# Kernel optimization log

Measured on AMD Instinct MI355X. Metric: run time of the kernel, lower is better.

## Reference

```python
import jax, jax.numpy as jnp
import numpy as np


def setup_inputs() -> dict:
    key = jax.random.key(0)
    ks = jax.random.split(key, 5)
    B, N, Fin, Fout = 8, 2048, 512, 512
    stdv = 1.0 / np.sqrt(Fout)
    w_stdv = 1.0 / np.sqrt(Fin)
    x = jax.random.normal(ks[0], (B, N, Fin), dtype=jnp.float32)
    weight = jax.random.uniform(ks[1], (Fin, Fout), dtype=jnp.float32, minval=-stdv, maxval=stdv)
    bias = jax.random.uniform(ks[2], (Fout,), dtype=jnp.float32, minval=-stdv, maxval=stdv)
    w_one = jax.random.uniform(ks[3], (Fin, Fin), dtype=jnp.float32, minval=-w_stdv, maxval=w_stdv)
    w_two = jax.random.uniform(ks[4], (Fin, Fin), dtype=jnp.float32, minval=-w_stdv, maxval=w_stdv)
    return {"x": x, "weight": weight, "bias": bias, "w_one": w_one, "w_two": w_two}


def reference(x, weight, bias, w_one, w_two):
    # x: [B, N, Fin]
    support = jnp.einsum('bnf,fo->bno', x, weight)          # [B, N, Fout]
    phi_one = jnp.einsum('ef,bnf->ben', w_one, x)           # [B, Fin, N]
    phi_two = jnp.einsum('ef,bnf->ben', w_two, x)           # [B, Fin, N]
    adj = jnp.einsum('ben,bem->bnm', phi_one, phi_two)      # [B, N, N]
    adj = jax.nn.softmax(adj, axis=1)                        # softmax over dim=1 (columns)
    out = jnp.einsum('bnm,bmo->bno', adj, support)           # [B, N, Fout]
    return out + bias
```

## Files before the change

### kernel.cpp

```cpp
#include <hip/hip_runtime.h>
#include <math.h>

#define BB 8
#define NN 2048
#define FF 512
#define LOG2E 1.4426950408889634f

typedef __attribute__((ext_vector_type(8))) short short8;
typedef __attribute__((ext_vector_type(4))) float floatx4;
typedef __attribute__((ext_vector_type(2))) float float2v;
typedef __attribute__((ext_vector_type(2))) __bf16 bf16x2;

__device__ __forceinline__ unsigned short f2bf(float f) {
    union { float f; unsigned u; } v; v.f = f;
    unsigned r = v.u + 0x7FFFu + ((v.u >> 16) & 1u);
    return (unsigned short)(r >> 16);
}

__device__ __forceinline__ float fexp2(float x) {
#if __has_builtin(__builtin_amdgcn_exp2f)
    return __builtin_amdgcn_exp2f(x);
#else
    return __expf(x * 0.69314718056f);
#endif
}

__device__ __forceinline__ void pk_store(unsigned short* p0, unsigned short* p1,
                                         float a, float b) {
    union { bf16x2 h; unsigned short s[2]; } u;
    float2v v; v.x = a; v.y = b;
    u.h = __builtin_convertvector(v, bf16x2);
    *p0 = u.s[0]; *p1 = u.s[1];
}

#define BAR() __builtin_amdgcn_s_barrier()
#define LGKM0() do { asm volatile("s_waitcnt lgkmcnt(0)" ::: "memory"); \
                     __builtin_amdgcn_sched_barrier(0); } while (0)
#define GLDS(src, dst) __builtin_amdgcn_global_load_lds( \
    (const __attribute__((address_space(1))) void*)(src), \
    (__attribute__((address_space(3))) void*)(dst), 16, 0, 0)
#define VMW(n) asm volatile("s_waitcnt vmcnt(" #n ")" ::: "memory")

template<int MODE>
__global__ __launch_bounds__(512) void gemm256(
    const unsigned short* __restrict__ A, const unsigned short* __restrict__ B,
    void* __restrict__ Cv, const float* __restrict__ bias, float* __restrict__ Dsum,
    int K, int a_ld, int b_ld, int ldc,
    long a_batch, long b_batch, long c_batch)
{
    constexpr int SLOT = 256 * 32;
    __shared__ __align__(16) unsigned short SH[8 * SLOT];

    const int tid  = threadIdx.x;
    const int wave = tid >> 6;
    const int lane = tid & 63;
    const int wr   = wave >> 2;
    const int wc   = wave & 3;
    const int fl   = lane & 15;
    const int quad = lane >> 4;

    const int gx = gridDim.x, gy = gridDim.y;
    int flat = blockIdx.x + gx * (blockIdx.y + gy * blockIdx.z);
    const int cpx = (gx * gy * gridDim.z) >> 3;
    flat = (flat & 7) * cpx + (flat >> 3);
    const int bx = flat % gx;
    const int rest = flat / gx;
    const int by = rest % gy;
    const int bz = rest / gy;

    const int m0 = by * 256;
    const int n0 = bx * 256;

    const unsigned short* Aptr = A + (long)bz * a_batch + (long)m0 * a_ld;
    const unsigned short* Bptr = B + (long)bz * b_batch + (long)n0 * b_ld;

    int offA[2], offB[2];
    #pragma unroll
    for (int i = 0; i < 2; ++i) {
        const int cl = i * 512 + tid;
        const int r = cl >> 2, s = cl & 3;
        const int c = s ^ ((r >> 1) & 3);
        offA[i] = r * a_ld + c * 8;
        offB[i] = r * b_ld + c * 8;
    }

    const int swz = (quad ^ ((fl >> 1) & 3)) * 8;
    const int aRd = (wr * 128 + fl) * 32 + swz;
    const int bRd = (wc * 64 + fl) * 32 + swz;

    auto sA = [&](int kh, int db, int kb) {
        #pragma unroll
        for (int i = 0; i < 2; ++i)
            GLDS(Aptr + kb + offA[i], &SH[(kh * 2 + db) * SLOT + (i * 512 + tid) * 8]);
    };
    auto sB = [&](int kh, int db, int kb) {
        #pragma unroll
        for (int i = 0; i < 2; ++i)
            GLDS(Bptr + kb + offB[i], &SH[(4 + kh * 2 + db) * SLOT + (i * 512 + tid) * 8]);
    };

    floatx4 acc[8][4] = {};
    short8 af[8], bf[2];

    auto RA = [&](int kh, int db) {
        const unsigned short* b = &SH[(kh * 2 + db) * SLOT + aRd];
        #pragma unroll
        for (int m = 0; m < 8; ++m) af[m] = *(const short8*)(b + m * 512);
    };
    auto RB = [&](int kh, int db, int nh) {
        const unsigned short* b = &SH[(4 + kh * 2 + db) * SLOT + bRd + nh * 1024];
        bf[0] = *(const short8*)(b);
        bf[1] = *(const short8*)(b + 512);
    };
    auto MC = [&](int nh) {
        __builtin_amdgcn_s_setprio(1);
        #pragma unroll
        for (int m = 0; m < 8; ++m) {
            acc[m][nh * 2]     = __builtin_amdgcn_mfma_f32_16x16x32_bf16(af[m], bf[0], acc[m][nh * 2], 0, 0, 0);
            acc[m][nh * 2 + 1] = __builtin_amdgcn_mfma_f32_16x16x32_bf16(af[m], bf[1], acc[m][nh * 2 + 1], 0, 0, 0);
        }
        __builtin_amdgcn_s_setprio(0);
    };

    const int nt = K >> 6;
    const int ni = nt >> 1;

    sA(0, 0, 0);  sB(0, 0, 0);  sA(1, 0, 32); sB(1, 0, 32);
    sA(0, 1, 64); sB(0, 1, 64); sA(1, 1, 96);
    VMW(6);
    BAR();

    for (int i = 0; i < ni; ++i) {
        const bool last = (i == ni - 1);
        const int kb1 = (2 * i + 1) * 64, kb2 = kb1 + 64, kb3 = kb2 + 64;

        RA(0, 0); RB(0, 0, 0);
        sB(1, 1, kb1 + 32);
        BAR(); LGKM0(); MC(0); BAR();
        RB(0, 0, 1);
        if (!last) sA(0, 0, kb2);
        BAR(); LGKM0(); MC(1); BAR();
        RA(1, 0); RB(1, 0, 0);
        if (!last) sB(0, 0, kb2);
        BAR(); LGKM0(); MC(0); BAR();
        RB(1, 0, 1);
        if (!last) { sA(1, 0, kb2 + 32); VMW(6); }
        else       { VMW(0); }
        BAR(); LGKM0(); MC(1); BAR();
        RA(0, 1); RB(0, 1, 0);
        if (!last) sB(1, 0, kb2 + 32);
        BAR(); LGKM0(); MC(0); BAR();
        RB(0, 1, 1);
        if (!last) sA(0, 1, kb3);
        BAR(); LGKM0(); MC(1); BAR();
        RA(1, 1); RB(1, 1, 0);
        if (!last) sB(0, 1, kb3);
        BAR(); LGKM0(); MC(0); BAR();
        RB(1, 1, 1);
        if (!last) { sA(1, 1, kb3 + 32); VMW(6); }
        BAR(); LGKM0(); MC(1); BAR();
    }

    const int wmg = m0 + wr * 128;
    const int wcol = wc * 64;

    if constexpr (MODE == 0) {
        float* Cb = (float*)Cv + (long)bz * c_batch;
        #pragma unroll
        for (int n = 0; n < 4; ++n) {
            const int ng = n0 + wcol + n * 16 + fl;
            const float badd = bias ? bias[ng] : 0.0f;
            #pragma unroll
            for (int m = 0; m < 8; ++m) {
                const int mg = wmg + m * 16 + quad * 4;
                #pragma unroll
                for (int r = 0; r < 4; ++r)
                    Cb[(long)(mg + r) * ldc + ng] = acc[m][n][r] + badd;
            }
        }
    } else {
        unsigned short* Cb = (unsigned short*)Cv + (long)bz * c_batch;
        if constexpr (MODE == 2) {
            float* Db = Dsum + (long)bz * NN;
            #pragma unroll
            for (int m = 0; m < 8; ++m)
                #pragma unroll
                for (int n = 0; n < 4; ++n)
                    #pragma unroll
                    for (int r = 0; r < 4; ++r)
                        acc[m][n][r] = fexp2(acc[m][n][r]);
            #pragma unroll
            for (int n = 0; n < 4; ++n) {
                float csum = 0.f;
                #pragma unroll
                for (int m = 0; m < 8; ++m)
                    csum += acc[m][n][0] + acc[m][n][1] + acc[m][n][2] + acc[m][n][3];
                csum += __shfl_xor(csum, 16);
                csum += __shfl_xor(csum, 32);
                if (quad == 0) atomicAdd(&Db[n0 + wcol + n * 16 + fl], csum);
            }
        }
        __syncthreads();
        #pragma unroll
        for (int m = 0; m < 8; ++m) {
            const int rowb = wr * 128 + m * 16 + quad * 4;
            #pragma unroll
            for (int n = 0; n < 4; ++n) {
                const int pc = (wcol + n * 16 + fl) ^ (quad << 4);
                #pragma unroll
                for (int r = 0; r < 4; ++r)
                    SH[(rowb + r) * 256 + pc] = f2bf(acc[m][n][r]);
            }
        }
        __syncthreads();
        #pragma unroll
        for (int k = 0; k < 16; ++k) {
            const int idx = k * 512 + tid;
            const int row = idx >> 5, c8 = (idx & 31) * 8;
            const int lcol = c8 ^ (((row >> 2) & 3) << 4);
            short8 vv = *(const short8*)&SH[row * 256 + lcol];
            *(short8*)&Cb[(long)(m0 + row) * ldc + n0 + c8] = vv;
        }
    }
}

__global__ __launch_bounds__(256) void convert_all(
    const float* __restrict__ x, const float* __restrict__ w1, const float* __restrict__ w2,
    unsigned short* __restrict__ xb, unsigned short* __restrict__ w1b, unsigned short* __restrict__ w2b)
{
    const long NX = (long)BB * NN * FF / 8;
    const long NW = (long)FF * FF / 8;
    long t = (long)blockIdx.x * 256 + threadIdx.x;
    const float* in; unsigned short* out; float sc = 1.0f;
    if (t < NX) { in = x; out = xb; }
    else if (t < NX + NW) { in = w1; out = w1b; t -= NX; sc = LOG2E; }
    else if (t < NX + 2 * NW) { in = w2; out = w2b; t -= NX + NW; }
    else return;
    const long i = t * 8;
    float4 a = *(const float4*)(in + i);
    float4 b = *(const float4*)(in + i + 4);
    union { bf16x2 h[4]; short8 s8; } u;
    float2v v;
    v.x = a.x * sc; v.y = a.y * sc; u.h[0] = __builtin_convertvector(v, bf16x2);
    v.x = a.z * sc; v.y = a.w * sc; u.h[1] = __builtin_convertvector(v, bf16x2);
    v.x = b.x * sc; v.y = b.y * sc; u.h[2] = __builtin_convertvector(v, bf16x2);
    v.x = b.z * sc; v.y = b.w * sc; u.h[3] = __builtin_convertvector(v, bf16x2);
    *(short8*)(out + i) = u.s8;
}

__global__ __launch_bounds__(256) void transpose_convert(
    const float* __restrict__ in, unsigned short* __restrict__ out, int dim)
{
    __shared__ float t[32][33];
    const int tx = threadIdx.x & 31, ty = threadIdx.x >> 5;
    const int x0 = blockIdx.x * 32, y0 = blockIdx.y * 32;
    #pragma unroll
    for (int k = 0; k < 32; k += 8)
        t[ty + k][tx] = in[(long)(y0 + ty + k) * dim + x0 + tx];
    __syncthreads();
    #pragma unroll
    for (int k = 0; k < 32; k += 8)
        out[(long)(x0 + ty + k) * dim + y0 + tx] = f2bf(t[tx][ty + k]);
}

__global__ __launch_bounds__(256) void zero_f32(float* __restrict__ p, long n)
{
    long i = (long)blockIdx.x * 256 + threadIdx.x;
    if (i < n) p[i] = 0.0f;
}

__global__ __launch_bounds__(256) void scale_transpose(
    const unsigned short* __restrict__ Call, const float* __restrict__ D,
    unsigned short* __restrict__ supT, int batch0)
{
    __shared__ float t[32][33];
    __shared__ float rD[32];
    const int tx = threadIdx.x & 31, ty = threadIdx.x >> 5;
    const int mt = blockIdx.x * 32, ot = blockIdx.y * 32;
    const int b = batch0 + blockIdx.z;
    const unsigned short* Cb = Call + (long)b * NN * 1536;
    unsigned short* Tb = supT + (long)b * NN * FF;
    if (threadIdx.x < 32) rD[threadIdx.x] = 1.0f / D[(long)b * NN + mt + threadIdx.x];
    __syncthreads();
    #pragma unroll
    for (int k = 0; k < 32; k += 8) {
        unsigned short u = Cb[(long)(mt + ty + k) * 1536 + 1024 + ot + tx];
        union { unsigned uu; float f; } cv; cv.uu = ((unsigned)u) << 16;
        t[ty + k][tx] = cv.f;
    }
    __syncthreads();
    #pragma unroll
    for (int k = 0; k < 32; k += 8)
        Tb[(long)(ot + ty + k) * NN + mt + tx] = f2bf(t[tx][ty + k] * rD[tx]);
}

extern "C" void kernel_launch(void* const* d_in, const int* in_sizes, int n_in,
                              void* d_out, int out_size, void* d_ws, size_t ws_size,
                              hipStream_t stream)
{
    const float* x      = (const float*)d_in[0];
    const float* weight = (const float*)d_in[1];
    const float* bias   = (const float*)d_in[2];
    const float* w_one  = (const float*)d_in[3];
    const float* w_two  = (const float*)d_in[4];
    float* out = (float*)d_out;

    const long NF  = (long)NN * FF;
    const long NN2 = (long)NN * NN;
    const long CROW = 1536;

    char* p = (char*)d_ws;
    unsigned short* xb    = (unsigned short*)p; p += (size_t)BB * NF * 2;
    unsigned short* Wall  = (unsigned short*)p; p += (size_t)CROW * FF * 2;
    unsigned short* Call  = (unsigned short*)p; p += (size_t)BB * NN * CROW * 2;
    unsigned short* supT  = (unsigned short*)p; p += (size_t)BB * NF * 2;
    float*          Dsum  = (float*)p;          p += (size_t)BB * NN * 4;
    unsigned short* E     = (unsigned short*)p;
    unsigned short* w1b = Wall;
    unsigned short* w2b = Wall + (size_t)FF * FF;
    unsigned short* wTb = Wall + (size_t)2 * FF * FF;

    const size_t fixed = (size_t)(p - (char*)d_ws);
    const bool full = ws_size >= fixed + (size_t)BB * NN2 * 2;

    dim3 blk(256), blk5(512);

    convert_all<<<dim3(4352), blk, 0, stream>>>(x, w_one, w_two, xb, w1b, w2b);
    transpose_convert<<<dim3(FF / 32, FF / 32), blk, 0, stream>>>(weight, wTb, FF);
    zero_f32<<<dim3((BB * NN) / 256), blk, 0, stream>>>(Dsum, BB * NN);

    gemm256<1><<<dim3(CROW / 256, NN / 256, BB), blk5, 0, stream>>>(
        xb, Wall, Call, nullptr, nullptr, FF,
        FF, FF, (int)CROW, NF, 0, NN * CROW);

    if (full) {
        gemm256<2><<<dim3(NN / 256, NN / 256, BB), blk5, 0, stream>>>(
            Call, Call + FF, E, nullptr, Dsum, FF,
            (int)CROW, (int)CROW, NN, NN * CROW, NN * CROW, NN2);
        scale_transpose<<<dim3(NN / 32, FF / 32, BB), blk, 0, stream>>>(Call, Dsum, supT, 0);
        gemm256<0><<<dim3(FF / 256, NN / 256, BB), blk5, 0, stream>>>(
            E, supT, out, bias, nullptr, NN,
            NN, NN, FF, NN2, NF, NF);
    } else {
        for (int b = 0; b < BB; ++b) {
            const unsigned short* Cb = Call + (size_t)b * NN * CROW;
            gemm256<2><<<dim3(NN / 256, NN / 256, 1), blk5, 0, stream>>>(
                Cb, Cb + FF, E, nullptr, Dsum + (size_t)b * NN, FF,
                (int)CROW, (int)CROW, NN, 0, 0, 0);
            scale_transpose<<<dim3(NN / 32, FF / 32, 1), blk, 0, stream>>>(Call, Dsum, supT, b);
            gemm256<0><<<dim3(FF / 256, NN / 256, 1), blk5, 0, stream>>>(
                E, supT + (size_t)b * NF, out + (size_t)b * NF, bias, nullptr, NN,
                NN, NN, FF, 0, 0, 0);
        }
    }
}
```

Measured before the change: 235.0 us.

## Fold w_one and w_two into one matrix and halve the projection GEMM

The two projections are combined algebraically: phi1^T·phi2 = x·(W1^T W2)·x^T, so a single 512x512 matrix V = W2^T-style product is precomputed. The attention-logit GEMM then multiplies x·V against x directly. This cuts the first projection GEMM from 1536 to 1024 output columns and shrinks the intermediate buffer. The GEMM template also gains an M_REP parameter, and the final output GEMM uses 128-row tiles to double its block count and improve occupancy. Risk: the extra bf16 rounding of V changes numerics slightly.

```diff
diff --git a/kernel.cpp b/kernel.cpp
--- a/kernel.cpp
+++ b/kernel.cpp
@@ -23,14 +23,6 @@
 #else
     return __expf(x * 0.69314718056f);
 #endif
-}
-
-__device__ __forceinline__ void pk_store(unsigned short* p0, unsigned short* p1,
-                                         float a, float b) {
-    union { bf16x2 h; unsigned short s[2]; } u;
-    float2v v; v.x = a; v.y = b;
-    u.h = __builtin_convertvector(v, bf16x2);
-    *p0 = u.s[0]; *p1 = u.s[1];
 }
 
 #define BAR() __builtin_amdgcn_s_barrier()
@@ -41,15 +33,18 @@
     (__attribute__((address_space(3))) void*)(dst), 16, 0, 0)
 #define VMW(n) asm volatile("s_waitcnt vmcnt(" #n ")" ::: "memory")
 
-template<int MODE>
+template<int M_REP, int MODE>
 __global__ __launch_bounds__(512) void gemm256(
     const unsigned short* __restrict__ A, const unsigned short* __restrict__ B,
     void* __restrict__ Cv, const float* __restrict__ bias, float* __restrict__ Dsum,
     int K, int a_ld, int b_ld, int ldc,
     long a_batch, long b_batch, long c_batch)
 {
-    constexpr int SLOT = 256 * 32;
-    __shared__ __align__(16) unsigned short SH[8 * SLOT];
+    constexpr int BM    = M_REP * 32;
+    constexpr int LA    = BM / 128;
+    constexpr int ASLOT = BM * 32;
+    constexpr int BSLOT = 256 * 32;
+    __shared__ __align__(16) unsigned short SH[4 * ASLOT + 4 * BSLOT];
 
     const int tid  = threadIdx.x;
     const int wave = tid >> 6;
@@ -62,60 +57,64 @@
     const int gx = gridDim.x, gy = gridDim.y;
     int flat = blockIdx.x + gx * (blockIdx.y + gy * blockIdx.z);
     const int cpx = (gx * gy * gridDim.z) >> 3;
-    flat = (flat & 7) * cpx + (flat >> 3);
+    if (cpx > 0) flat = (flat & 7) * cpx + (flat >> 3);
     const int bx = flat % gx;
     const int rest = flat / gx;
     const int by = rest % gy;
     const int bz = rest / gy;
 
-    const int m0 = by * 256;
+    const int m0 = by * BM;
     const int n0 = bx * 256;
 
     const unsigned short* Aptr = A + (long)bz * a_batch + (long)m0 * a_ld;
     const unsigned short* Bptr = B + (long)bz * b_batch + (long)n0 * b_ld;
 
-    int offA[2], offB[2];
+    int offA[LA], offB[2];
+    #pragma unroll
+    for (int i = 0; i < LA; ++i) {
+        const int cl = i * 512 + tid;
+        const int r = cl >> 2, s = cl & 3;
+        offA[i] = r * a_ld + (s ^ ((r >> 1) & 3)) * 8;
+    }
     #pragma unroll
     for (int i = 0; i < 2; ++i) {
         const int cl = i * 512 + tid;
         const int r = cl >> 2, s = cl & 3;
-        const int c = s ^ ((r >> 1) & 3);
-        offA[i] = r * a_ld + c * 8;
-        offB[i] = r * b_ld + c * 8;
+        offB[i] = r * b_ld + (s ^ ((r >> 1) & 3)) * 8;
     }
 
     const int swz = (quad ^ ((fl >> 1) & 3)) * 8;
-    const int aRd = (wr * 128 + fl) * 32 + swz;
+    const int aRd = (wr * (M_REP * 16) + fl) * 32 + swz;
     const int bRd = (wc * 64 + fl) * 32 + swz;
 
     auto sA = [&](int kh, int db, int kb) {
         #pragma unroll
+        for (int i = 0; i < LA; ++i)
+            GLDS(Aptr + kb + offA[i], &SH[(kh * 2 + db) * ASLOT + (i * 512 + tid) * 8]);
+    };
+    auto sB = [&](int kh, int db, int kb) {
+        #pragma unroll
         for (int i = 0; i < 2; ++i)
-            GLDS(Aptr + kb + offA[i], &SH[(kh * 2 + db) * SLOT + (i * 512 + tid) * 8]);
-    };
-    auto sB = [&](int kh, int db, int kb) {
-        #pragma unroll
-        for (int i = 0; i < 2; ++i)
-            GLDS(Bptr + kb + offB[i], &SH[(4 + kh * 2 + db) * SLOT + (i * 512 + tid) * 8]);
-    };
-
-    floatx4 acc[8][4] = {};
-    short8 af[8], bf[2];
+            GLDS(Bptr + kb + offB[i], &SH[4 * ASLOT + (kh * 2 + db) * BSLOT + (i * 512 + tid) * 8]);
+    };
+
+    floatx4 acc[M_REP][4] = {};
+    short8 af[M_REP], bf[2];
 
     auto RA = [&](int kh, int db) {
-        const unsigned short* b = &SH[(kh * 2 + db) * SLOT + aRd];
-        #pragma unroll
-        for (int m = 0; m < 8; ++m) af[m] = *(const short8*)(b + m * 512);
+        const unsigned short* b = &SH[(kh * 2 + db) * ASLOT + aRd];
+        #pragma unroll
+        for (int m = 0; m < M_REP; ++m) af[m] = *(const short8*)(b + m * 512);
     };
     auto RB = [&](int kh, int db, int nh) {
-        const unsigned short* b = &SH[(4 + kh * 2 + db) * SLOT + bRd + nh * 1024];
+        const unsigned short* b = &SH[4 * ASLOT + (kh * 2 + db) * BSLOT + bRd + nh * 1024];
         bf[0] = *(const short8*)(b);
         bf[1] = *(const short8*)(b + 512);
     };
     auto MC = [&](int nh) {
         __builtin_amdgcn_s_setprio(1);
         #pragma unroll
-        for (int m = 0; m < 8; ++m) {
+        for (int m = 0; m < M_REP; ++m) {
             acc[m][nh * 2]     = __builtin_amdgcn_mfma_f32_16x16x32_bf16(af[m], bf[0], acc[m][nh * 2], 0, 0, 0);
             acc[m][nh * 2 + 1] = __builtin_amdgcn_mfma_f32_16x16x32_bf16(af[m], bf[1], acc[m][nh * 2 + 1], 0, 0, 0);
         }
@@ -127,7 +126,7 @@
 
     sA(0, 0, 0);  sB(0, 0, 0);  sA(1, 0, 32); sB(1, 0, 32);
     sA(0, 1, 64); sB(0, 1, 64); sA(1, 1, 96);
-    VMW(6);
+    if constexpr (LA == 2) VMW(6); else VMW(4);
     BAR();
 
     for (int i = 0; i < ni; ++i) {
@@ -144,8 +143,12 @@
         if (!last) sB(0, 0, kb2);
         BAR(); LGKM0(); MC(0); BAR();
         RB(1, 0, 1);
-        if (!last) { sA(1, 0, kb2 + 32); VMW(6); }
-        else       { VMW(0); }
+        if (!last) {
+            sA(1, 0, kb2 + 32);
+            if constexpr (LA == 2) VMW(6); else VMW(4);
+        } else {
+            VMW(0);
+        }
         BAR(); LGKM0(); MC(1); BAR();
         RA(0, 1); RB(0, 1, 0);
         if (!last) sB(1, 0, kb2 + 32);
@@ -157,11 +160,14 @@
         if (!last) sB(0, 1, kb3);
         BAR(); LGKM0(); MC(0); BAR();
         RB(1, 1, 1);
-        if (!last) { sA(1, 1, kb3 + 32); VMW(6); }
+        if (!last) {
+            sA(1, 1, kb3 + 32);
+            if constexpr (LA == 2) VMW(6); else VMW(4);
+        }
         BAR(); LGKM0(); MC(1); BAR();
     }
 
-    const int wmg = m0 + wr * 128;
+    const int wmg = m0 + wr * (M_REP * 16);
     const int wcol = wc * 64;
 
     if constexpr (MODE == 0) {
@@ -171,7 +177,7 @@
             const int ng = n0 + wcol + n * 16 + fl;
             const float badd = bias ? bias[ng] : 0.0f;
             #pragma unroll
-            for (int m = 0; m < 8; ++m) {
+            for (int m = 0; m < M_REP; ++m) {
                 const int mg = wmg + m * 16 + quad * 4;
                 #pragma unroll
                 for (int r = 0; r < 4; ++r)
@@ -183,7 +189,7 @@
         if constexpr (MODE == 2) {
             float* Db = Dsum + (long)bz * NN;
             #pragma unroll
-            for (int m = 0; m < 8; ++m)
+            for (int m = 0; m < M_REP; ++m)
                 #pragma unroll
                 for (int n = 0; n < 4; ++n)
                     #pragma unroll
@@ -193,7 +199,7 @@
             for (int n = 0; n < 4; ++n) {
                 float csum = 0.f;
                 #pragma unroll
-                for (int m = 0; m < 8; ++m)
+                for (int m = 0; m < M_REP; ++m)
                     csum += acc[m][n][0] + acc[m][n][1] + acc[m][n][2] + acc[m][n][3];
                 csum += __shfl_xor(csum, 16);
                 csum += __shfl_xor(csum, 32);
@@ -202,8 +208,8 @@
         }
         __syncthreads();
         #pragma unroll
-        for (int m = 0; m < 8; ++m) {
-            const int rowb = wr * 128 + m * 16 + quad * 4;
+        for (int m = 0; m < M_REP; ++m) {
+            const int rowb = wr * (M_REP * 16) + m * 16 + quad * 4;
             #pragma unroll
             for (int n = 0; n < 4; ++n) {
                 const int pc = (wcol + n * 16 + fl) ^ (quad << 4);
@@ -214,7 +220,7 @@
         }
         __syncthreads();
         #pragma unroll
-        for (int k = 0; k < 16; ++k) {
+        for (int k = 0; k < M_REP * 2; ++k) {
             const int idx = k * 512 + tid;
             const int row = idx >> 5, c8 = (idx & 31) * 8;
             const int lcol = c8 ^ (((row >> 2) & 3) << 4);
@@ -224,32 +230,23 @@
     }
 }
 
-__global__ __launch_bounds__(256) void convert_all(
-    const float* __restrict__ x, const float* __restrict__ w1, const float* __restrict__ w2,
-    unsigned short* __restrict__ xb, unsigned short* __restrict__ w1b, unsigned short* __restrict__ w2b)
-{
-    const long NX = (long)BB * NN * FF / 8;
-    const long NW = (long)FF * FF / 8;
-    long t = (long)blockIdx.x * 256 + threadIdx.x;
-    const float* in; unsigned short* out; float sc = 1.0f;
-    if (t < NX) { in = x; out = xb; }
-    else if (t < NX + NW) { in = w1; out = w1b; t -= NX; sc = LOG2E; }
-    else if (t < NX + 2 * NW) { in = w2; out = w2b; t -= NX + NW; }
-    else return;
-    const long i = t * 8;
-    float4 a = *(const float4*)(in + i);
-    float4 b = *(const float4*)(in + i + 4);
+__global__ __launch_bounds__(256) void convert_x(
+    const float* __restrict__ x, unsigned short* __restrict__ xb)
+{
+    const long i = ((long)blockIdx.x * 256 + threadIdx.x) * 8;
+    float4 a = *(const float4*)(x + i);
+    float4 b = *(const float4*)(x + i + 4);
     union { bf16x2 h[4]; short8 s8; } u;
     float2v v;
-    v.x = a.x * sc; v.y = a.y * sc; u.h[0] = __builtin_convertvector(v, bf16x2);
-    v.x = a.z * sc; v.y = a.w * sc; u.h[1] = __builtin_convertvector(v, bf16x2);
-    v.x = b.x * sc; v.y = b.y * sc; u.h[2] = __builtin_convertvector(v, bf16x2);
-    v.x = b.z * sc; v.y = b.w * sc; u.h[3] = __builtin_convertvector(v, bf16x2);
-    *(short8*)(out + i) = u.s8;
+    v.x = a.x; v.y = a.y; u.h[0] = __builtin_convertvector(v, bf16x2);
+    v.x = a.z; v.y = a.w; u.h[1] = __builtin_convertvector(v, bf16x2);
+    v.x = b.x; v.y = b.y; u.h[2] = __builtin_convertvector(v, bf16x2);
+    v.x = b.z; v.y = b.w; u.h[3] = __builtin_convertvector(v, bf16x2);
+    *(short8*)(xb + i) = u.s8;
 }
 
 __global__ __launch_bounds__(256) void transpose_convert(
-    const float* __restrict__ in, unsigned short* __restrict__ out, int dim)
+    const float* __restrict__ in, unsigned short* __restrict__ out, int dim, float sc)
 {
     __shared__ float t[32][33];
     const int tx = threadIdx.x & 31, ty = threadIdx.x >> 5;
@@ -260,7 +257,7 @@
     __syncthreads();
     #pragma unroll
     for (int k = 0; k < 32; k += 8)
-        out[(long)(x0 + ty + k) * dim + y0 + tx] = f2bf(t[tx][ty + k]);
+        out[(long)(x0 + ty + k) * dim + y0 + tx] = f2bf(t[tx][ty + k] * sc);
 }
 
 __global__ __launch_bounds__(256) void zero_f32(float* __restrict__ p, long n)
@@ -278,13 +275,13 @@
     const int tx = threadIdx.x & 31, ty = threadIdx.x >> 5;
     const int mt = blockIdx.x * 32, ot = blockIdx.y * 32;
     const int b = batch0 + blockIdx.z;
-    const unsigned short* Cb = Call + (long)b * NN * 1536;
+    const unsigned short* Cb = Call + (long)b * NN * 1024;
     unsigned short* Tb = supT + (long)b * NN * FF;
     if (threadIdx.x < 32) rD[threadIdx.x] = 1.0f / D[(long)b * NN + mt + threadIdx.x];
     __syncthreads();
     #pragma unroll
     for (int k = 0; k < 32; k += 8) {
-        unsigned short u = Cb[(long)(mt + ty + k) * 1536 + 1024 + ot + tx];
+        unsigned short u = Cb[(long)(mt + ty + k) * 1024 + 512 + ot + tx];
         union { unsigned uu; float f; } cv; cv.uu = ((unsigned)u) << 16;
         t[ty + k][tx] = cv.f;
     }
@@ -307,48 +304,55 @@
 
     const long NF  = (long)NN * FF;
     const long NN2 = (long)NN * NN;
-    const long CROW = 1536;
+    const long CROW = 1024;
 
     char* p = (char*)d_ws;
     unsigned short* xb    = (unsigned short*)p; p += (size_t)BB * NF * 2;
-    unsigned short* Wall  = (unsigned short*)p; p += (size_t)CROW * FF * 2;
+    unsigned short* Wg1   = (unsigned short*)p; p += (size_t)1024 * FF * 2;
+    unsigned short* w1T   = (unsigned short*)p; p += (size_t)FF * FF * 2;
+    unsigned short* w2T   = (unsigned short*)p; p += (size_t)FF * FF * 2;
     unsigned short* Call  = (unsigned short*)p; p += (size_t)BB * NN * CROW * 2;
     unsigned short* supT  = (unsigned short*)p; p += (size_t)BB * NF * 2;
     float*          Dsum  = (float*)p;          p += (size_t)BB * NN * 4;
     unsigned short* E     = (unsigned short*)p;
-    unsigned short* w1b = Wall;
-    unsigned short* w2b = Wall + (size_t)FF * FF;
-    unsigned short* wTb = Wall + (size_t)2 * FF * FF;
+    unsigned short* Vw  = Wg1;
+    unsigned short* wTb = Wg1 + (size_t)FF * FF;
 
     const size_t fixed = (size_t)(p - (char*)d_ws);
     const bool full = ws_size >= fixed + (size_t)BB * NN2 * 2;
 
     dim3 blk(256), blk5(512);
 
-    convert_all<<<dim3(4352), blk, 0, stream>>>(x, w_one, w_two, xb, w1b, w2b);
-    transpose_convert<<<dim3(FF / 32, FF / 32), blk, 0, stream>>>(weight, wTb, FF);
+    convert_x<<<dim3((unsigned)(BB * NF / (256 * 8))), blk, 0, stream>>>(x, xb);
+    transpose_convert<<<dim3(FF / 32, FF / 32), blk, 0, stream>>>(w_one, w1T, FF, LOG2E);
+    transpose_convert<<<dim3(FF / 32, FF / 32), blk, 0, stream>>>(w_two, w2T, FF, 1.0f);
+    transpose_convert<<<dim3(FF / 32, FF / 32), blk, 0, stream>>>(weight, wTb, FF, 1.0f);
     zero_f32<<<dim3((BB * NN) / 256), blk, 0, stream>>>(Dsum, BB * NN);
 
-    gemm256<1><<<dim3(CROW / 256, NN / 256, BB), blk5, 0, stream>>>(
-        xb, Wall, Call, nullptr, nullptr, FF,
+    gemm256<8, 1><<<dim3(FF / 256, FF / 256, 1), blk5, 0, stream>>>(
+        w2T, w1T, Vw, nullptr, nullptr, FF,
+        FF, FF, FF, 0, 0, 0);
+
+    gemm256<8, 1><<<dim3(1024 / 256, NN / 256, BB), blk5, 0, stream>>>(
+        xb, Wg1, Call, nullptr, nullptr, FF,
         FF, FF, (int)CROW, NF, 0, NN * CROW);
 
     if (full) {
-        gemm256<2><<<dim3(NN / 256, NN / 256, BB), blk5, 0, stream>>>(
-            Call, Call + FF, E, nullptr, Dsum, FF,
-            (int)CROW, (int)CROW, NN, NN * CROW, NN * CROW, NN2);
+        gemm256<8, 2><<<dim3(NN / 256, NN / 256, BB), blk5, 0, stream>>>(
+            Call, xb, E, nullptr, Dsum, FF,
+            (int)CROW, FF, NN, NN * CROW, NF, NN2);
         scale_transpose<<<dim3(NN / 32, FF / 32, BB), blk, 0, stream>>>(Call, Dsum, supT, 0);
-        gemm256<0><<<dim3(FF / 256, NN / 256, BB), blk5, 0, stream>>>(
+        gemm256<4, 0><<<dim3(FF / 256, NN / 128, BB), blk5, 0, stream>>>(
             E, supT, out, bias, nullptr, NN,
             NN, NN, FF, NN2, NF, NF);
     } else {
         for (int b = 0; b < BB; ++b) {
             const unsigned short* Cb = Call + (size_t)b * NN * CROW;
-            gemm256<2><<<dim3(NN / 256, NN / 256, 1), blk5, 0, stream>>>(
-                Cb, Cb + FF, E, nullptr, Dsum + (size_t)b * NN, FF,
-                (int)CROW, (int)CROW, NN, 0, 0, 0);
+            gemm256<8, 2><<<dim3(NN / 256, NN / 256, 1), blk5, 0, stream>>>(
+                Cb, xb + (size_t)b * NF, E, nullptr, Dsum + (size_t)b * NN, FF,
+                (int)CROW, FF, NN, 0, 0, 0);
             scale_transpose<<<dim3(NN / 32, FF / 32, 1), blk, 0, stream>>>(Call, Dsum, supT, b);
-            gemm256<0><<<dim3(FF / 256, NN / 256, 1), blk5, 0, stream>>>(
+            gemm256<4, 0><<<dim3(FF / 256, NN / 128, 1), blk5, 0, stream>>>(
                 E, supT + (size_t)b * NF, out + (size_t)b * NF, bias, nullptr, NN,
                 NN, NN, FF, 0, 0, 0);
         }
```

Measured after the change: 224.6 us. -4.4%, faster.
